# Optimization experiments

Hardware: AMD Instinct MI355X
Metric: run time of the kernel (lower is better)

## Reference

```python
import jax, jax.numpy as jnp
import numpy as np

N, C, H, W = 1, 1, 4096, 4096

def setup_inputs() -> dict:
    key = jax.random.key(0)
    x = jax.random.normal(key, (N, C, H, W), dtype=jnp.float32)
    return {"x": x}

def reference(x):
    # torch.median returns the lower of the two middle values for even counts:
    # take the k-th smallest with k = (n-1)//2.
    n = x.size
    median = jnp.sort(x.reshape(-1))[(n - 1) // 2]
    # threshold everything below the median to zero
    thresholded = jnp.where(x < median, jnp.float32(0.0), x)
    # 7x7 max pool, stride 1, padding 3 (torch pads with -inf for max pool)
    pooled = jax.lax.reduce_window(
        thresholded,
        -jnp.inf,
        jax.lax.max,
        window_dimensions=(1, 1, 7, 7),
        window_strides=(1, 1, 1, 1),
        padding=[(0, 0), (0, 0), (3, 3), (3, 3)],
    )
    # In the original, gather(flatten(thresholded), max_indices) == pooled,
    # so binarize where the thresholded value equals its local window max.
    binarized = jnp.where(thresholded == pooled, jnp.float32(1.0), jnp.float32(0.0))
    return binarized * x
```

## Files before the change

### kernel.cpp

```cpp
#include <hip/hip_runtime.h>
#include <math.h>

#define IMG_H 4096
#define IMG_W 4096
#define TS 64
#define HALO 3
#define TW 70
#define THS 71
#define HMS 65
#define NBINS 4096
#define CBLK 1024
#define CAPB 4096
#define WLO (-0.001953125f)
#define WHI ( 0.001953125f)
#define MCAP 1024
#define NSUB 2048

struct SelState { float median; };

__device__ __forceinline__ unsigned f2u(float f) {
    unsigned b = __float_as_uint(f);
    unsigned mask = (unsigned)(-(int)(b >> 31)) | 0x80000000u;
    return b ^ mask;
}
__device__ __forceinline__ float u2f(unsigned u) {
    unsigned mask = (u >> 31) ? 0x80000000u : 0xFFFFFFFFu;
    return __uint_as_float(u ^ mask);
}

__device__ __forceinline__ int val_bin(float v) {
    float t = (v + 4.0f) * 512.0f;
    int b = (int)t;
    b = b < 0 ? 0 : b;
    b = b > (NBINS - 1) ? (NBINS - 1) : b;
    return b;
}

__device__ __forceinline__ int sub_bin(float v) {
    float t = (v - WLO) * (float)(NSUB * 256);
    int b = (int)t;
    b = b < 0 ? 0 : b;
    b = b > (NSUB - 1) ? (NSUB - 1) : b;
    return b;
}

__global__ __launch_bounds__(512, 8) void count_compact(
    const float4* __restrict__ x4, int n4,
    unsigned* __restrict__ belowCnt,
    unsigned* __restrict__ candCnt,
    unsigned* __restrict__ candA)
{
    __shared__ unsigned buf[CAPB];
    __shared__ unsigned wred[8];
    __shared__ unsigned lcnt;
    const int t = threadIdx.x;
    if (t == 0) lcnt = 0;
    __syncthreads();

    unsigned below = 0;
    const int idx = blockIdx.x * 512 + t;
    const int stride = CBLK * 512;

    if (n4 == 8 * stride) {
        float4 v[8];
        #pragma unroll
        for (int j = 0; j < 8; j++) v[j] = x4[idx + j * stride];
        #pragma unroll
        for (int j = 0; j < 8; j++) {
            float vs[4] = {v[j].x, v[j].y, v[j].z, v[j].w};
            #pragma unroll
            for (int u = 0; u < 4; u++) {
                float vv = vs[u];
                below += (vv < WLO) ? 1u : 0u;
                if (vv >= WLO && vv < WHI) {
                    unsigned p = atomicAdd(&lcnt, 1u);
                    if (p < CAPB) buf[p] = f2u(vv);
                }
            }
        }
    } else {
        for (int i = idx; i < n4; i += stride) {
            float4 v = x4[i];
            float vs[4] = {v.x, v.y, v.z, v.w};
            #pragma unroll
            for (int u = 0; u < 4; u++) {
                float vv = vs[u];
                below += (vv < WLO) ? 1u : 0u;
                if (vv >= WLO && vv < WHI) {
                    unsigned p = atomicAdd(&lcnt, 1u);
                    if (p < CAPB) buf[p] = f2u(vv);
                }
            }
        }
    }

    #pragma unroll
    for (int off = 32; off >= 1; off >>= 1) below += __shfl_down(below, off, 64);
    if ((t & 63) == 0) wred[t >> 6] = below;
    __syncthreads();
    if (t == 0) {
        unsigned tot = 0;
        #pragma unroll
        for (int w = 0; w < 8; w++) tot += wred[w];
        belowCnt[blockIdx.x] = tot;
        candCnt[blockIdx.x] = lcnt;
    }
    unsigned m = lcnt; if (m > CAPB) m = CAPB;
    const unsigned gbase = (unsigned)blockIdx.x * CAPB;
    for (unsigned i = t; i < m; i += 512) candA[gbase + i] = buf[i];
}

__global__ __launch_bounds__(1024) void finalize_fb(
    const float4* __restrict__ x4, int n4, unsigned K,
    const unsigned* __restrict__ belowCnt,
    const unsigned* __restrict__ candCnt,
    const unsigned* __restrict__ candA,
    unsigned* __restrict__ candB,
    SelState* __restrict__ st)
{
    __shared__ unsigned hist[NSUB];
    __shared__ unsigned mem[MCAP];
    __shared__ unsigned lh[NBINS];
    __shared__ unsigned wsA[16], wsB[16], wsC[16];
    __shared__ unsigned s_below, s_M, s_ovf, s_sb, s_kr2, mcnt;
    __shared__ unsigned s_bin, s_krem, s_m, s_pref, s_kr;
    const int t = threadIdx.x;
    const unsigned lane = t & 63, wid = t >> 6;

    const unsigned cc = candCnt[t];
    unsigned bsum = belowCnt[t];
    unsigned csum = cc;
    unsigned osum = (cc > CAPB) ? 1u : 0u;
    #pragma unroll
    for (int off = 32; off >= 1; off >>= 1) {
        bsum += __shfl_down(bsum, off, 64);
        csum += __shfl_down(csum, off, 64);
        osum += __shfl_down(osum, off, 64);
    }
    if (lane == 0) { wsA[wid] = bsum; wsB[wid] = csum; wsC[wid] = osum; }
    if (t == 0) mcnt = 0;
    __syncthreads();
    if (t == 0) {
        unsigned b = 0, c = 0, o = 0;
        #pragma unroll
        for (int w = 0; w < 16; w++) { b += wsA[w]; c += wsB[w]; o += wsC[w]; }
        s_below = b; s_M = c; s_ovf = o;
    }
    __syncthreads();

    const unsigned below = s_below, M = s_M;
    bool resolved = false;
    if (s_ovf == 0u && K >= below && (K - below) < M) {
        const unsigned kRem = K - below;
        for (int i = t; i < NSUB; i += 1024) hist[i] = 0;
        __syncthreads();

        const unsigned base = (unsigned)t * CAPB;
        for (unsigned i = 0; i < cc; i++)
            atomicAdd(&hist[sub_bin(u2f(candA[base + i]))], 1u);
        __syncthreads();

        unsigned d0 = hist[t * 2], d1 = hist[t * 2 + 1];
        unsigned loc2 = d0 + d1;
        unsigned s2 = loc2;
        #pragma unroll
        for (int off = 1; off < 64; off <<= 1) {
            unsigned u = __shfl_up(s2, off, 64);
            if (lane >= off) s2 += u;
        }
        if (lane == 63) wsA[wid] = s2;
        __syncthreads();
        unsigned base2 = 0;
        for (unsigned w = 0; w < wid; w++) base2 += wsA[w];
        unsigned excl2 = base2 + s2 - loc2;
        if (kRem >= excl2 && kRem < excl2 + loc2) {
            if (kRem < excl2 + d0) { s_sb = (unsigned)(t * 2);     s_kr2 = kRem - excl2; }
            else                   { s_sb = (unsigned)(t * 2 + 1); s_kr2 = kRem - excl2 - d0; }
        }
        __syncthreads();

        const int sb = (int)s_sb;
        for (unsigned i = 0; i < cc; i++) {
            unsigned key = candA[base + i];
            if (sub_bin(u2f(key)) == sb) {
                unsigned p = atomicAdd(&mcnt, 1u);
                if (p < MCAP) mem[p] = key;
            }
        }
        __syncthreads();
        if (mcnt <= MCAP) {
            const unsigned m = mcnt, kr2 = s_kr2;
            if ((unsigned)t < m) {
                unsigned ku = mem[t], c = 0, e = 0;
                for (unsigned j = 0; j < m; j++) {
                    unsigned kj = mem[j];
                    c += (kj < ku);
                    e += (kj == ku);
                }
                if (c <= kr2 && kr2 < c + e) st->median = u2f(ku);
            }
            resolved = true;
        }
    }
    if (resolved) return;

    __syncthreads();
    for (int i = t; i < NBINS; i += 1024) lh[i] = 0;
    __syncthreads();
    for (int i = t; i < n4; i += 1024) {
        float4 v = x4[i];
        atomicAdd(&lh[val_bin(v.x)], 1u);
        atomicAdd(&lh[val_bin(v.y)], 1u);
        atomicAdd(&lh[val_bin(v.z)], 1u);
        atomicAdd(&lh[val_bin(v.w)], 1u);
    }
    __syncthreads();

    {
        unsigned cb[4];
        unsigned local = 0;
        #pragma unroll
        for (int j = 0; j < 4; j++) { cb[j] = lh[t * 4 + j]; local += cb[j]; }
        unsigned s = local;
        #pragma unroll
        for (int off = 1; off < 64; off <<= 1) {
            unsigned u = __shfl_up(s, off, 64);
            if (lane >= off) s += u;
        }
        if (lane == 63) wsA[wid] = s;
        __syncthreads();
        unsigned base = 0;
        for (unsigned w = 0; w < wid; w++) base += wsA[w];
        unsigned excl = base + s - local;
        if (K >= excl && K < excl + local) {
            unsigned cum = excl;
            #pragma unroll
            for (int j = 0; j < 4; j++) {
                if (K < cum + cb[j]) { s_bin = (unsigned)(t * 4 + j); s_krem = K - cum; break; }
                cum += cb[j];
            }
        }
        if (t == 0) s_m = 0;
        __syncthreads();
    }

    {
        const int b = (int)s_bin;
        for (int i = t; i < n4; i += 1024) {
            float4 v = x4[i];
            float vs[4] = {v.x, v.y, v.z, v.w};
            #pragma unroll
            for (int j = 0; j < 4; j++) {
                if (val_bin(vs[j]) == b) {
                    unsigned p = atomicAdd(&s_m, 1u);
                    candB[p] = f2u(vs[j]);
                }
            }
        }
        __syncthreads();
    }

    const int M2 = (int)s_m;
    if (t == 0) { s_pref = 0; s_kr = s_krem; }
    for (int p = 0; p < 3; p++) {
        const int shift = (p == 0) ? 21 : ((p == 1) ? 10 : 0);
        const int bits  = (p == 2) ? 10 : 11;
        const int nb    = 1 << bits;
        for (int i = t; i < nb; i += 1024) lh[i] = 0;
        __syncthreads();
        const unsigned pref = s_pref;
        for (int i = t; i < M2; i += 1024) {
            unsigned u = candB[i];
            bool ok = (p == 0) || ((u >> ((p == 1) ? 21 : 10)) == pref);
            if (ok) atomicAdd(&lh[(u >> shift) & (unsigned)(nb - 1)], 1u);
        }
        __syncthreads();
        const int P = nb >> 10;
        unsigned c0 = lh[t * (P ? P : 1)];
        unsigned c1 = (P == 2) ? lh[t * 2 + 1] : 0u;
        if (P == 0) { c0 = (t < nb) ? lh[t] : 0u; c1 = 0u; }
        unsigned local = c0 + c1;
        unsigned s = local;
        #pragma unroll
        for (int off = 1; off < 64; off <<= 1) {
            unsigned u = __shfl_up(s, off, 64);
            if (lane >= off) s += u;
        }
        if (lane == 63) wsA[wid] = s;
        __syncthreads();
        unsigned base = 0;
        for (unsigned w = 0; w < wid; w++) base += wsA[w];
        unsigned excl = base + s - local;
        unsigned kRem2 = s_kr;
        __syncthreads();
        if (kRem2 >= excl && kRem2 < excl + local) {
            if (P == 2) {
                if (kRem2 < excl + c0) { s_pref = (pref << bits) | (unsigned)(t * 2);     s_kr = kRem2 - excl; }
                else                   { s_pref = (pref << bits) | (unsigned)(t * 2 + 1); s_kr = kRem2 - excl - c0; }
            } else {
                s_pref = (pref << bits) | (unsigned)t;
                s_kr = kRem2 - excl;
            }
        }
        __syncthreads();
    }
    if (t == 0) st->median = u2f(s_pref);
}

__global__ __launch_bounds__(512) void nms_kernel(
    const float* __restrict__ x, float* __restrict__ out,
    const SelState* __restrict__ st)
{
    __shared__ float th[TW * THS];
    __shared__ float hm[TW * HMS];

    const float med = st->median;
    const float NEGINF = -__builtin_inff();
    const int bx = blockIdx.x, by = blockIdx.y;
    const int gy0 = by * TS - HALO;
    const int gcol0 = bx * TS - 4;

    if (bx >= 1 && bx <= (IMG_W / TS) - 2 && by >= 1 && by <= (IMG_H / TS) - 2) {
        #pragma unroll
        for (int k = 0; k < 3; k++) {
            int task = threadIdx.x + k * 512;
            if (task < TW * 18) {
                int r = task / 18, q = task - r * 18;
                const float4 v = *(const float4*)&x[(gy0 + r) * IMG_W + (gcol0 + q * 4)];
                float vs[4] = {v.x, v.y, v.z, v.w};
                #pragma unroll
                for (int cmp = 0; cmp < 4; cmp++) {
                    int c = q * 4 - 1 + cmp;
                    if ((unsigned)c < (unsigned)TW)
                        th[r * THS + c] = (vs[cmp] < med) ? 0.0f : vs[cmp];
                }
            }
        }
    } else {
        for (int task = threadIdx.x; task < TW * 18; task += 512) {
            int r = task / 18, q = task - r * 18;
            int gy = gy0 + r;
            int gxb = gcol0 + q * 4;
            bool rowok = (gy >= 0 && gy < IMG_H);
            float vs[4];
            if (rowok && gxb >= 0 && gxb + 4 <= IMG_W) {
                float4 v = *(const float4*)&x[gy * IMG_W + gxb];
                vs[0] = v.x; vs[1] = v.y; vs[2] = v.z; vs[3] = v.w;
            } else if (rowok) {
                #pragma unroll
                for (int cmp = 0; cmp < 4; cmp++) {
                    int gx = gxb + cmp;
                    vs[cmp] = (gx >= 0 && gx < IMG_W) ? x[gy * IMG_W + gx] : NEGINF;
                }
            } else {
                vs[0] = vs[1] = vs[2] = vs[3] = NEGINF;
            }
            #pragma unroll
            for (int cmp = 0; cmp < 4; cmp++) {
                int c = q * 4 - 1 + cmp;
                if ((unsigned)c < (unsigned)TW) {
                    float v = vs[cmp];
                    v = (v == NEGINF) ? v : ((v < med) ? 0.0f : v);
                    th[r * THS + c] = v;
                }
            }
        }
    }
    __syncthreads();

    for (int task = threadIdx.x; task < TW * 8; task += 512) {
        int r = task % TW;
        int c0 = (task / TW) * 8;
        float w[7];
        #pragma unroll
        for (int i = 0; i < 14; i++) {
            w[i % 7] = th[r * THS + c0 + i];
            if (i >= 6) {
                float m = w[0];
                #pragma unroll
                for (int k = 1; k < 7; k++) m = fmaxf(m, w[k]);
                hm[r * HMS + c0 + i - 6] = m;
            }
        }
    }
    __syncthreads();

    {
        const int c = threadIdx.x & 63;
        const int rr0 = (threadIdx.x >> 6) * 8;
        float w[7];
        #pragma unroll
        for (int i = 0; i < 14; i++) {
            w[i % 7] = hm[(rr0 + i) * HMS + c];
            if (i >= 6) {
                int R = rr0 + i - 6;
                float m = w[0];
                #pragma unroll
                for (int k = 1; k < 7; k++) m = fmaxf(m, w[k]);
                float t = th[(R + HALO) * THS + (c + HALO)];
                int gy = by * TS + R;
                int gx = bx * TS + c;
                float o = 0.0f;
                if (t == m) {
                    o = (t != 0.0f) ? t : x[gy * IMG_W + gx];
                }
                out[gy * IMG_W + gx] = o;
            }
        }
    }
}

extern "C" void kernel_launch(void* const* d_in, const int* in_sizes, int n_in,
                              void* d_out, int out_size, void* d_ws, size_t ws_size,
                              hipStream_t stream)
{
    const float* x = (const float*)d_in[0];
    float* out = (float*)d_out;
    const int n = in_sizes[0];
    const unsigned K = (unsigned)((n - 1) / 2);

    char* ws = (char*)d_ws;
    SelState* st       = (SelState*)ws;
    unsigned* belowCnt = (unsigned*)(ws + 1024);
    unsigned* candCnt  = (unsigned*)(ws + 1024 + 4096);
    unsigned* candA    = (unsigned*)(ws + ws_size / 2);

    const int n4 = n / 4;
    count_compact<<<CBLK, 512, 0, stream>>>((const float4*)x, n4,
                                            belowCnt, candCnt, candA);
    finalize_fb<<<1, 1024, 0, stream>>>((const float4*)x, n4, K,
                                        belowCnt, candCnt, candA,
                                        (unsigned*)d_out, st);
    dim3 fg(IMG_W / TS, IMG_H / TS);
    nms_kernel<<<fg, 512, 0, stream>>>(x, out, st);
}
```

Before: 152.5 us.

## Coalesce candidate reads in median finalize with per-wave register prefetch

In the single-block finalize kernel, each wave now loads the first 64 candidates of 64 producer blocks, one per lane, into registers. The loads are issued upfront and coalesced, replacing each thread's serial strided walk over its own block's candidates. Candidates beyond the first 64 per block are still read serially. The histogram clear moves into the first barrier phase, saving a barrier. Holding 64 keys per thread raises register pressure in a 1024-thread block and may cause spills.

```diff
diff --git a/kernel.cpp b/kernel.cpp
--- a/kernel.cpp
+++ b/kernel.cpp
@@ -121,43 +121,58 @@
     __shared__ unsigned hist[NSUB];
     __shared__ unsigned mem[MCAP];
     __shared__ unsigned lh[NBINS];
+    __shared__ unsigned ccs[CBLK];
     __shared__ unsigned wsA[16], wsB[16], wsC[16];
     __shared__ unsigned s_below, s_M, s_ovf, s_sb, s_kr2, mcnt;
     __shared__ unsigned s_bin, s_krem, s_m, s_pref, s_kr;
     const int t = threadIdx.x;
     const unsigned lane = t & 63, wid = t >> 6;
 
-    const unsigned cc = candCnt[t];
-    unsigned bsum = belowCnt[t];
-    unsigned csum = cc;
-    unsigned osum = (cc > CAPB) ? 1u : 0u;
+    const unsigned rbase = wid * 64u;
+    unsigned key[64];
     #pragma unroll
-    for (int off = 32; off >= 1; off >>= 1) {
-        bsum += __shfl_down(bsum, off, 64);
-        csum += __shfl_down(csum, off, 64);
-        osum += __shfl_down(osum, off, 64);
-    }
-    if (lane == 0) { wsA[wid] = bsum; wsB[wid] = csum; wsC[wid] = osum; }
-    if (t == 0) mcnt = 0;
-    __syncthreads();
-    if (t == 0) {
-        unsigned b = 0, c = 0, o = 0;
-        #pragma unroll
-        for (int w = 0; w < 16; w++) { b += wsA[w]; c += wsB[w]; o += wsC[w]; }
-        s_below = b; s_M = c; s_ovf = o;
-    }
-    __syncthreads();
+    for (int g = 0; g < 64; g++)
+        key[g] = candA[(rbase + (unsigned)g) * CAPB + lane];
+
+    {
+        const unsigned cc = candCnt[t];
+        ccs[t] = cc;
+        unsigned bsum = belowCnt[t];
+        unsigned csum = cc;
+        unsigned osum = (cc > CAPB) ? 1u : 0u;
+        #pragma unroll
+        for (int off = 32; off >= 1; off >>= 1) {
+            bsum += __shfl_down(bsum, off, 64);
+            csum += __shfl_down(csum, off, 64);
+            osum += __shfl_down(osum, off, 64);
+        }
+        if (lane == 0) { wsA[wid] = bsum; wsB[wid] = csum; wsC[wid] = osum; }
+        if (t == 0) mcnt = 0;
+        for (int i = t; i < NSUB; i += 1024) hist[i] = 0;
+        __syncthreads();
+        if (t == 0) {
+            unsigned b = 0, c = 0, o = 0;
+            #pragma unroll
+            for (int w = 0; w < 16; w++) { b += wsA[w]; c += wsB[w]; o += wsC[w]; }
+            s_below = b; s_M = c; s_ovf = o;
+        }
+        __syncthreads();
+    }
 
     const unsigned below = s_below, M = s_M;
     bool resolved = false;
     if (s_ovf == 0u && K >= below && (K - below) < M) {
         const unsigned kRem = K - below;
-        for (int i = t; i < NSUB; i += 1024) hist[i] = 0;
-        __syncthreads();
-
-        const unsigned base = (unsigned)t * CAPB;
-        for (unsigned i = 0; i < cc; i++)
-            atomicAdd(&hist[sub_bin(u2f(candA[base + i]))], 1u);
+
+        #pragma unroll
+        for (int g = 0; g < 64; g++)
+            if (lane < ccs[rbase + (unsigned)g])
+                atomicAdd(&hist[sub_bin(u2f(key[g]))], 1u);
+        for (int r = t; r < CBLK; r += 1024) {
+            const unsigned cc = ccs[r];
+            for (unsigned j = 64; j < cc; j++)
+                atomicAdd(&hist[sub_bin(u2f(candA[(unsigned)r * CAPB + j]))], 1u);
+        }
         __syncthreads();
 
         unsigned d0 = hist[t * 2], d1 = hist[t * 2 + 1];
@@ -180,11 +195,22 @@
         __syncthreads();
 
         const int sb = (int)s_sb;
-        for (unsigned i = 0; i < cc; i++) {
-            unsigned key = candA[base + i];
-            if (sub_bin(u2f(key)) == sb) {
+        #pragma unroll
+        for (int g = 0; g < 64; g++) {
+            if (lane < ccs[rbase + (unsigned)g] &&
+                sub_bin(u2f(key[g])) == sb) {
                 unsigned p = atomicAdd(&mcnt, 1u);
-                if (p < MCAP) mem[p] = key;
+                if (p < MCAP) mem[p] = key[g];
+            }
+        }
+        for (int r = t; r < CBLK; r += 1024) {
+            const unsigned cc = ccs[r];
+            for (unsigned j = 64; j < cc; j++) {
+                unsigned k2 = candA[(unsigned)r * CAPB + j];
+                if (sub_bin(u2f(k2)) == sb) {
+                    unsigned p = atomicAdd(&mcnt, 1u);
+                    if (p < MCAP) mem[p] = k2;
+                }
             }
         }
         __syncthreads();
@@ -296,7 +322,7 @@
         if (kRem2 >= excl && kRem2 < excl + local) {
             if (P == 2) {
                 if (kRem2 < excl + c0) { s_pref = (pref << bits) | (unsigned)(t * 2);     s_kr = kRem2 - excl; }
-                else                   { s_pref = (pref << bits) | (unsigned)(t * 2 + 1); s_kr = kRem2 - excl - c0; }
+                else                  { s_pref = (pref << bits) | (unsigned)(t * 2 + 1); s_kr = kRem2 - excl - c0; }
             } else {
                 s_pref = (pref << bits) | (unsigned)t;
                 s_kr = kRem2 - excl;
```

Result: faster. 146.6 us (-3.8%).
